# Kernel tuning notes

Measured on AMD Instinct MI355X. Metric: run time of the kernel, lower is better.

Reference implementation:

```python
import jax, jax.numpy as jnp
import numpy as np

# Module hyperparameters (match init_kwargs)
RES_SCALE = 1.0
INPUT_SCALE = 1.0
LEAK = 0.9  # leak_rate
SEQ_LEN = 4096
INPUT_SIZE = 128
RES_SIZE = 2048
BIAS_SCALE = 0.4


def setup_inputs() -> dict:
    key = jax.random.key(0)
    k1, k2, k3, k4 = jax.random.split(key, 4)
    return {
        "input_data": jax.random.normal(k1, (SEQ_LEN, INPUT_SIZE), jnp.float32),
        "W_in": jax.random.normal(k2, (RES_SIZE, INPUT_SIZE), jnp.float32),
        "W_res": jax.random.normal(k3, (RES_SIZE, RES_SIZE), jnp.float32),
        "bias": BIAS_SCALE * jax.random.normal(k4, (RES_SIZE,), jnp.float32),
    }


def reference(input_data, W_in, W_res, bias):
    """ESN forward with f=erf, random_projection='gpu', no initial_state.

    x[i] = (1-leak)*x[i-1]
           + leak * erf(res_scale*W_res@x[i-1] + input_scale*W_in@u[i] + bias) / sqrt(res_size)
    Returns states of shape (seq_len, res_size).
    """
    res_size = W_res.shape[0]
    inv_sqrt = jnp.asarray(1.0 / np.sqrt(res_size), input_data.dtype)
    # Batch the input projection into one GEMM: (T, res)
    proj_in = INPUT_SCALE * input_data @ W_in.T + bias

    def step(s, u_t):
        pre = RES_SCALE * (W_res @ s) + u_t
        s_new = (1.0 - LEAK) * s + LEAK * jax.lax.erf(pre) * inv_sqrt
        return s_new, s_new

    s0 = jnp.zeros((res_size,), input_data.dtype)
    _, xs = jax.lax.scan(step, s0, proj_in)
    return xs
```

## Files before the change

kernel.cpp:

```cpp
#include <hip/hip_runtime.h>
#include <hip/hip_cooperative_groups.h>
#include <math.h>

typedef unsigned int u32x4 __attribute__((ext_vector_type(4)));

constexpr int T = 4096;
constexpr int R = 2048;
constexpr int J = 128;
constexpr float ONE_MINUS_LEAK = 0.1f;
constexpr float LEAK = 0.9f;
constexpr float INV_SQRT_R = 0.022097086912079608f;

constexpr int NWG  = 64;
constexpr int NREP = 2;

__global__ __launch_bounds__(256) void esn_proj_kernel(
    const float* __restrict__ U, const float* __restrict__ Win,
    const float* __restrict__ bias, float* __restrict__ out)
{
    __shared__ float As[16][129];
    __shared__ float Bs[16][129];
    const int tb = blockIdx.x * 16;
    const int rb = blockIdx.y * 16;
    const int tid = threadIdx.x;

    for (int i = tid; i < 16 * J; i += 256) {
        int r = i >> 7, c = i & 127;
        As[r][c] = U[(size_t)(tb + r) * J + c];
        Bs[r][c] = Win[(size_t)(rb + r) * J + c];
    }
    __syncthreads();

    const int ti = tid >> 4;
    const int rj = tid & 15;
    float acc = 0.f;
#pragma unroll
    for (int k = 0; k < J; ++k) acc = fmaf(As[ti][k], Bs[rj][k], acc);
    out[(size_t)(tb + ti) * R + (rb + rj)] = acc + bias[rb + rj];
}

__global__ __launch_bounds__(512) void esn_recur_kernel(
    const float* __restrict__ Wres, float* __restrict__ out,
    unsigned* __restrict__ slots )
{
    const int wg   = blockIdx.x;
    const int tid  = threadIdx.x;
    const int wv   = tid >> 6;
    const int lane = tid & 63;
    const int rowbase = wg * 32 + wv * 4;
    const int rep  = wg & (NREP - 1);

    float w[4][32];
#pragma unroll
    for (int j = 0; j < 4; ++j) {
        const float* wr = Wres + (size_t)(rowbase + j) * R + lane;
#pragma unroll
        for (int k = 0; k < 32; ++k) w[j][k] = wr[k * 64];
    }

    __shared__ __align__(16) float xs[2][R];
    float xold = 0.f;
    long  spin = 0;

    for (int t = 0; t < T; ++t) {
        float proj = (lane < 4) ? out[(size_t)t * R + rowbase + lane] : 0.f;

        const unsigned* p =
            slots + ((size_t)((t & 1) * NREP + rep)) * R + 4 * tid;
        const unsigned want = (unsigned)t & 0xFFu;
        u32x4 v;
        while (true) {
            asm volatile(
                "global_load_dwordx4 %0, %1, off sc0 sc1\n\t"
                "s_waitcnt vmcnt(0)"
                : "=&v"(v) : "v"(p) : "memory");
            if ((v[0] & 0xFFu) == want && (v[1] & 0xFFu) == want &&
                (v[2] & 0xFFu) == want && (v[3] & 0xFFu) == want) break;
            if (++spin > (1L << 26)) break;
        }
        float4 xv = make_float4(__uint_as_float(v[0] & 0xFFFFFF00u),
                                __uint_as_float(v[1] & 0xFFFFFF00u),
                                __uint_as_float(v[2] & 0xFFFFFF00u),
                                __uint_as_float(v[3] & 0xFFFFFF00u));
        *(float4*)&xs[t & 1][4 * tid] = xv;
        __syncthreads();

        const float* x = xs[t & 1];
        float xr[32];
#pragma unroll
        for (int k = 0; k < 32; ++k) xr[k] = x[k * 64 + lane];

        float mysum = 0.f;
#pragma unroll
        for (int j = 0; j < 4; ++j) {
            float a0 = 0.f, a1 = 0.f, a2 = 0.f, a3 = 0.f;
#pragma unroll
            for (int k = 0; k < 8; ++k) {
                a0 = fmaf(w[j][4 * k + 0], xr[4 * k + 0], a0);
                a1 = fmaf(w[j][4 * k + 1], xr[4 * k + 1], a1);
                a2 = fmaf(w[j][4 * k + 2], xr[4 * k + 2], a2);
                a3 = fmaf(w[j][4 * k + 3], xr[4 * k + 3], a3);
            }
            float acc = (a0 + a1) + (a2 + a3);
#pragma unroll
            for (int off = 32; off > 0; off >>= 1)
                acc += __shfl_xor(acc, off);
            if (lane == j) mysum = acc;
        }

        if (lane < 4) {
            const float pre  = mysum + proj;
            const float xnew = ONE_MINUS_LEAK * xold +
                               LEAK * erff(pre) * INV_SQRT_R;
            xold = xnew;
            const unsigned bits =
                ((__float_as_uint(xnew) + 0x80u) & 0xFFFFFF00u) |
                ((unsigned)(t + 1) & 0xFFu);
            const size_t pb = (size_t)(((t + 1) & 1) * NREP) * R
                            + rowbase + lane;
#pragma unroll
            for (int g = 0; g < NREP; ++g)
                __hip_atomic_store(&slots[pb + (size_t)g * R], bits,
                                   __ATOMIC_RELAXED, __HIP_MEMORY_SCOPE_AGENT);
            out[(size_t)t * R + rowbase + lane] = xnew;
        }
    }
}

extern "C" void kernel_launch(void* const* d_in, const int* in_sizes, int n_in,
                              void* d_out, int out_size, void* d_ws, size_t ws_size,
                              hipStream_t stream) {
    const float* U    = (const float*)d_in[0];
    const float* Win  = (const float*)d_in[1];
    const float* Wres = (const float*)d_in[2];
    const float* bias = (const float*)d_in[3];
    float* out = (float*)d_out;
    unsigned* slots = (unsigned*)d_ws;

    hipMemsetAsync(slots, 0, (size_t)2 * NREP * R * sizeof(unsigned), stream);

    dim3 pgrid(T / 16, R / 16);
    esn_proj_kernel<<<pgrid, dim3(256), 0, stream>>>(U, Win, bias, out);

    void* args[] = { (void*)&Wres, (void*)&out, (void*)&slots };
    hipLaunchCooperativeKernel((const void*)esn_recur_kernel,
                               dim3(NWG), dim3(512), args, 0, stream);
}
```

Measured before the change: 11.96 ms.

## Poll full state vector per wave directly into registers, dropping LDS and barrier

```diff
diff --git a/kernel.cpp b/kernel.cpp
--- a/kernel.cpp
+++ b/kernel.cpp
@@ -1,8 +1,6 @@
 #include <hip/hip_runtime.h>
 #include <hip/hip_cooperative_groups.h>
 #include <math.h>
-
-typedef unsigned int u32x4 __attribute__((ext_vector_type(4)));
 
 constexpr int T = 4096;
 constexpr int R = 2048;
@@ -58,37 +56,71 @@
         for (int k = 0; k < 32; ++k) w[j][k] = wr[k * 64];
     }
 
-    __shared__ __align__(16) float xs[2][R];
     float xold = 0.f;
     long  spin = 0;
 
     for (int t = 0; t < T; ++t) {
         float proj = (lane < 4) ? out[(size_t)t * R + rowbase + lane] : 0.f;
 
-        const unsigned* p =
-            slots + ((size_t)((t & 1) * NREP + rep)) * R + 4 * tid;
+        const unsigned* base =
+            slots + ((size_t)((t & 1) * NREP + rep)) * R + lane;
+        const unsigned* p0 = base;
+        const unsigned* p1 = base + 1024;
         const unsigned want = (unsigned)t & 0xFFu;
-        u32x4 v;
+        unsigned v[32];
         while (true) {
             asm volatile(
-                "global_load_dwordx4 %0, %1, off sc0 sc1\n\t"
+                "global_load_dword %0,  %32, off sc0 sc1\n\t"
+                "global_load_dword %1,  %32, off offset:256 sc0 sc1\n\t"
+                "global_load_dword %2,  %32, off offset:512 sc0 sc1\n\t"
+                "global_load_dword %3,  %32, off offset:768 sc0 sc1\n\t"
+                "global_load_dword %4,  %32, off offset:1024 sc0 sc1\n\t"
+                "global_load_dword %5,  %32, off offset:1280 sc0 sc1\n\t"
+                "global_load_dword %6,  %32, off offset:1536 sc0 sc1\n\t"
+                "global_load_dword %7,  %32, off offset:1792 sc0 sc1\n\t"
+                "global_load_dword %8,  %32, off offset:2048 sc0 sc1\n\t"
+                "global_load_dword %9,  %32, off offset:2304 sc0 sc1\n\t"
+                "global_load_dword %10, %32, off offset:2560 sc0 sc1\n\t"
+                "global_load_dword %11, %32, off offset:2816 sc0 sc1\n\t"
+                "global_load_dword %12, %32, off offset:3072 sc0 sc1\n\t"
+                "global_load_dword %13, %32, off offset:3328 sc0 sc1\n\t"
+                "global_load_dword %14, %32, off offset:3584 sc0 sc1\n\t"
+                "global_load_dword %15, %32, off offset:3840 sc0 sc1\n\t"
+                "global_load_dword %16, %33, off sc0 sc1\n\t"
+                "global_load_dword %17, %33, off offset:256 sc0 sc1\n\t"
+                "global_load_dword %18, %33, off offset:512 sc0 sc1\n\t"
+                "global_load_dword %19, %33, off offset:768 sc0 sc1\n\t"
+                "global_load_dword %20, %33, off offset:1024 sc0 sc1\n\t"
+                "global_load_dword %21, %33, off offset:1280 sc0 sc1\n\t"
+                "global_load_dword %22, %33, off offset:1536 sc0 sc1\n\t"
+                "global_load_dword %23, %33, off offset:1792 sc0 sc1\n\t"
+                "global_load_dword %24, %33, off offset:2048 sc0 sc1\n\t"
+                "global_load_dword %25, %33, off offset:2304 sc0 sc1\n\t"
+                "global_load_dword %26, %33, off offset:2560 sc0 sc1\n\t"
+                "global_load_dword %27, %33, off offset:2816 sc0 sc1\n\t"
+                "global_load_dword %28, %33, off offset:3072 sc0 sc1\n\t"
+                "global_load_dword %29, %33, off offset:3328 sc0 sc1\n\t"
+                "global_load_dword %30, %33, off offset:3584 sc0 sc1\n\t"
+                "global_load_dword %31, %33, off offset:3840 sc0 sc1\n\t"
                 "s_waitcnt vmcnt(0)"
-                : "=&v"(v) : "v"(p) : "memory");
-            if ((v[0] & 0xFFu) == want && (v[1] & 0xFFu) == want &&
-                (v[2] & 0xFFu) == want && (v[3] & 0xFFu) == want) break;
+                : "=&v"(v[0]),  "=&v"(v[1]),  "=&v"(v[2]),  "=&v"(v[3]),
+                  "=&v"(v[4]),  "=&v"(v[5]),  "=&v"(v[6]),  "=&v"(v[7]),
+                  "=&v"(v[8]),  "=&v"(v[9]),  "=&v"(v[10]), "=&v"(v[11]),
+                  "=&v"(v[12]), "=&v"(v[13]), "=&v"(v[14]), "=&v"(v[15]),
+                  "=&v"(v[16]), "=&v"(v[17]), "=&v"(v[18]), "=&v"(v[19]),
+                  "=&v"(v[20]), "=&v"(v[21]), "=&v"(v[22]), "=&v"(v[23]),
+                  "=&v"(v[24]), "=&v"(v[25]), "=&v"(v[26]), "=&v"(v[27]),
+                  "=&v"(v[28]), "=&v"(v[29]), "=&v"(v[30]), "=&v"(v[31])
+                : "v"(p0), "v"(p1)
+                : "memory");
+            bool ok = true;
+#pragma unroll
+            for (int k = 0; k < 32; ++k) ok &= ((v[k] & 0xFFu) == want);
+            if (ok) break;
             if (++spin > (1L << 26)) break;
         }
-        float4 xv = make_float4(__uint_as_float(v[0] & 0xFFFFFF00u),
-                                __uint_as_float(v[1] & 0xFFFFFF00u),
-                                __uint_as_float(v[2] & 0xFFFFFF00u),
-                                __uint_as_float(v[3] & 0xFFFFFF00u));
-        *(float4*)&xs[t & 1][4 * tid] = xv;
-        __syncthreads();
-
-        const float* x = xs[t & 1];
-        float xr[32];
 #pragma unroll
-        for (int k = 0; k < 32; ++k) xr[k] = x[k * 64 + lane];
+        for (int k = 0; k < 32; ++k) v[k] &= 0xFFFFFF00u;
 
         float mysum = 0.f;
 #pragma unroll
@@ -96,10 +128,10 @@
             float a0 = 0.f, a1 = 0.f, a2 = 0.f, a3 = 0.f;
 #pragma unroll
             for (int k = 0; k < 8; ++k) {
-                a0 = fmaf(w[j][4 * k + 0], xr[4 * k + 0], a0);
-                a1 = fmaf(w[j][4 * k + 1], xr[4 * k + 1], a1);
-                a2 = fmaf(w[j][4 * k + 2], xr[4 * k + 2], a2);
-                a3 = fmaf(w[j][4 * k + 3], xr[4 * k + 3], a3);
+                a0 = fmaf(w[j][4 * k + 0], __uint_as_float(v[4 * k + 0]), a0);
+                a1 = fmaf(w[j][4 * k + 1], __uint_as_float(v[4 * k + 1]), a1);
+                a2 = fmaf(w[j][4 * k + 2], __uint_as_float(v[4 * k + 2]), a2);
+                a3 = fmaf(w[j][4 * k + 3], __uint_as_float(v[4 * k + 3]), a3);
             }
             float acc = (a0 + a1) + (a2 + a3);
 #pragma unroll
```

Result: slower. 17.63 ms (+47.4%).

## Fuse input projection into recurrent kernel and race duplicate workgroup instances

Applied to the files above, without the earlier changes.

```diff
diff --git a/kernel.cpp b/kernel.cpp
--- a/kernel.cpp
+++ b/kernel.cpp
@@ -11,43 +11,20 @@
 constexpr float LEAK = 0.9f;
 constexpr float INV_SQRT_R = 0.022097086912079608f;
 
-constexpr int NWG  = 64;
-constexpr int NREP = 2;
-
-__global__ __launch_bounds__(256) void esn_proj_kernel(
-    const float* __restrict__ U, const float* __restrict__ Win,
-    const float* __restrict__ bias, float* __restrict__ out)
-{
-    __shared__ float As[16][129];
-    __shared__ float Bs[16][129];
-    const int tb = blockIdx.x * 16;
-    const int rb = blockIdx.y * 16;
-    const int tid = threadIdx.x;
-
-    for (int i = tid; i < 16 * J; i += 256) {
-        int r = i >> 7, c = i & 127;
-        As[r][c] = U[(size_t)(tb + r) * J + c];
-        Bs[r][c] = Win[(size_t)(rb + r) * J + c];
-    }
-    __syncthreads();
-
-    const int ti = tid >> 4;
-    const int rj = tid & 15;
-    float acc = 0.f;
-#pragma unroll
-    for (int k = 0; k < J; ++k) acc = fmaf(As[ti][k], Bs[rj][k], acc);
-    out[(size_t)(tb + ti) * R + (rb + rj)] = acc + bias[rb + rj];
-}
+constexpr int NINST = 2;
+constexpr int NWG   = 64 * NINST;
+constexpr int NREP  = 2;
 
 __global__ __launch_bounds__(512) void esn_recur_kernel(
-    const float* __restrict__ Wres, float* __restrict__ out,
-    unsigned* __restrict__ slots )
+    const float* __restrict__ U, const float* __restrict__ Win,
+    const float* __restrict__ Wres, const float* __restrict__ bias,
+    float* __restrict__ out, unsigned* __restrict__ slots )
 {
     const int wg   = blockIdx.x;
     const int tid  = threadIdx.x;
     const int wv   = tid >> 6;
     const int lane = tid & 63;
-    const int rowbase = wg * 32 + wv * 4;
+    const int rowbase = (wg & 63) * 32 + wv * 4;
     const int rep  = wg & (NREP - 1);
 
     float w[4][32];
@@ -57,13 +34,28 @@
 #pragma unroll
         for (int k = 0; k < 32; ++k) w[j][k] = wr[k * 64];
     }
+    float w2a[4], w2b[4];
+#pragma unroll
+    for (int j = 0; j < 4; ++j) {
+        const float* wi = Win + (size_t)(rowbase + j) * J;
+        w2a[j] = wi[lane];
+        w2b[j] = wi[64 + lane];
+    }
+    const float biasr = (lane < 4) ? bias[rowbase + lane] : 0.f;
 
     __shared__ __align__(16) float xs[2][R];
+    __shared__ __align__(16) float ul[2][J];
+    __shared__ int s_abort;
+    if (tid == 0) s_abort = 0;
+    __syncthreads();
+
     float xold = 0.f;
     long  spin = 0;
 
     for (int t = 0; t < T; ++t) {
-        float proj = (lane < 4) ? out[(size_t)t * R + rowbase + lane] : 0.f;
+        if (tid < 32)
+            *(float4*)&ul[t & 1][4 * tid] =
+                *(const float4*)(U + (size_t)t * J + 4 * tid);
 
         const unsigned* p =
             slots + ((size_t)((t & 1) * NREP + rep)) * R + 4 * tid;
@@ -74,9 +66,15 @@
                 "global_load_dwordx4 %0, %1, off sc0 sc1\n\t"
                 "s_waitcnt vmcnt(0)"
                 : "=&v"(v) : "v"(p) : "memory");
-            if ((v[0] & 0xFFu) == want && (v[1] & 0xFFu) == want &&
-                (v[2] & 0xFFu) == want && (v[3] & 0xFFu) == want) break;
-            if (++spin > (1L << 26)) break;
+            unsigned d0 = (v[0] - want) & 0xFFu, d1 = (v[1] - want) & 0xFFu;
+            unsigned d2 = (v[2] - want) & 0xFFu, d3 = (v[3] - want) & 0xFFu;
+            if ((d0 | d1 | d2 | d3) == 0u) break;
+            if (((d0 && d0 < 128u) | (d1 && d1 < 128u) |
+                 (d2 && d2 < 128u) | (d3 && d3 < 128u)) ||
+                ++spin > (1L << 26)) {
+                s_abort = 1;
+                break;
+            }
         }
         float4 xv = make_float4(__uint_as_float(v[0] & 0xFFFFFF00u),
                                 __uint_as_float(v[1] & 0xFFFFFF00u),
@@ -84,13 +82,15 @@
                                 __uint_as_float(v[3] & 0xFFFFFF00u));
         *(float4*)&xs[t & 1][4 * tid] = xv;
         __syncthreads();
+        if (s_abort) return;
 
         const float* x = xs[t & 1];
         float xr[32];
 #pragma unroll
         for (int k = 0; k < 32; ++k) xr[k] = x[k * 64 + lane];
+        const float uu0 = ul[t & 1][lane];
+        const float uu1 = ul[t & 1][64 + lane];
 
-        float mysum = 0.f;
 #pragma unroll
         for (int j = 0; j < 4; ++j) {
             float a0 = 0.f, a1 = 0.f, a2 = 0.f, a3 = 0.f;
@@ -101,28 +101,30 @@
                 a2 = fmaf(w[j][4 * k + 2], xr[4 * k + 2], a2);
                 a3 = fmaf(w[j][4 * k + 3], xr[4 * k + 3], a3);
             }
+            a0 = fmaf(w2a[j], uu0, a0);
+            a1 = fmaf(w2b[j], uu1, a1);
             float acc = (a0 + a1) + (a2 + a3);
 #pragma unroll
             for (int off = 32; off > 0; off >>= 1)
                 acc += __shfl_xor(acc, off);
-            if (lane == j) mysum = acc;
-        }
 
-        if (lane < 4) {
-            const float pre  = mysum + proj;
-            const float xnew = ONE_MINUS_LEAK * xold +
-                               LEAK * erff(pre) * INV_SQRT_R;
-            xold = xnew;
-            const unsigned bits =
-                ((__float_as_uint(xnew) + 0x80u) & 0xFFFFFF00u) |
-                ((unsigned)(t + 1) & 0xFFu);
-            const size_t pb = (size_t)(((t + 1) & 1) * NREP) * R
-                            + rowbase + lane;
+            if (lane == j) {
+                const float pre  = acc + biasr;
+                const float xnew = ONE_MINUS_LEAK * xold +
+                                   LEAK * erff(pre) * INV_SQRT_R;
+                xold = xnew;
+                const unsigned bits =
+                    ((__float_as_uint(xnew) + 0x80u) & 0xFFFFFF00u) |
+                    ((unsigned)(t + 1) & 0xFFu);
+                const size_t pb = (size_t)(((t + 1) & 1) * NREP) * R
+                                + rowbase + j;
 #pragma unroll
-            for (int g = 0; g < NREP; ++g)
-                __hip_atomic_store(&slots[pb + (size_t)g * R], bits,
-                                   __ATOMIC_RELAXED, __HIP_MEMORY_SCOPE_AGENT);
-            out[(size_t)t * R + rowbase + lane] = xnew;
+                for (int g = 0; g < NREP; ++g)
+                    __hip_atomic_store(&slots[pb + (size_t)g * R], bits,
+                                       __ATOMIC_RELAXED,
+                                       __HIP_MEMORY_SCOPE_AGENT);
+                out[(size_t)t * R + rowbase + j] = xnew;
+            }
         }
     }
 }
@@ -139,10 +141,8 @@
 
     hipMemsetAsync(slots, 0, (size_t)2 * NREP * R * sizeof(unsigned), stream);
 
-    dim3 pgrid(T / 16, R / 16);
-    esn_proj_kernel<<<pgrid, dim3(256), 0, stream>>>(U, Win, bias, out);
-
-    void* args[] = { (void*)&Wres, (void*)&out, (void*)&slots };
+    void* args[] = { (void*)&U, (void*)&Win, (void*)&Wres, (void*)&bias,
+                     (void*)&out, (void*)&slots };
     hipLaunchCooperativeKernel((const void*)esn_recur_kernel,
                                dim3(NWG), dim3(512), args, 0, stream);
 }
```

Result: slower. 20.84 ms (+74.3%).
